# Kernel optimization log

Measured on AMD Instinct MI355X. Metric: run time of the kernel, lower is better.

The kernel has to match this reference:

```python
import jax, jax.numpy as jnp
import numpy as np

EMBED_DIM = 768
NUM_HEADS = 12
KEY_DIM = EMBED_DIM // NUM_HEADS
B, S = 2, 2048

def _xavier(key, shape):
    # xavier_uniform over last-two dims (fan_in = shape[-2], fan_out = shape[-1])
    fan_in, fan_out = shape[-2], shape[-1]
    limit = jnp.sqrt(6.0 / (fan_in + fan_out)).astype(jnp.float32)
    return jax.random.uniform(key, shape, jnp.float32, -limit, limit)

def setup_inputs() -> dict:
    key = jax.random.key(0)
    kq, kk, kv, kwq, kwk, kwv, kw, km = jax.random.split(key, 8)
    q = jax.random.normal(kq, (B, S, EMBED_DIM), jnp.float32)
    k = jax.random.normal(kk, (B, S, EMBED_DIM), jnp.float32)
    v = jax.random.normal(kv, (B, S, EMBED_DIM), jnp.float32)
    # per-head projection weights stacked: [H, E, Dk]
    Wq = _xavier(kwq, (NUM_HEADS, EMBED_DIM, KEY_DIM))
    Wk = _xavier(kwk, (NUM_HEADS, EMBED_DIM, KEY_DIM))
    Wv = _xavier(kwv, (NUM_HEADS, EMBED_DIM, KEY_DIM))
    W = _xavier(kw, (EMBED_DIM, EMBED_DIM))
    mask = jax.random.randint(km, (B, 1, S, S), 0, 2).astype(jnp.int32)
    return {"q": q, "k": k, "v": v, "mask": mask, "Wq": Wq, "Wk": Wk, "Wv": Wv, "W": W}

def reference(q, k, v, mask, Wq, Wk, Wv, W):
    scale = 1.0 / jnp.sqrt(jnp.asarray(KEY_DIM, q.dtype))
    Q = jnp.einsum('bse,hed->bhsd', q, Wq)  # [B,H,S,Dk]
    K = jnp.einsum('bse,hed->bhsd', k, Wk)
    V = jnp.einsum('bse,hed->bhsd', v, Wv)
    Z = jnp.einsum('bhsd,bhtd->bhst', Q, K) * scale  # [B,H,S,S]
    Z = jnp.where(mask == 0, jnp.asarray(-1e9, Z.dtype), Z)
    score = jax.nn.softmax(Z, axis=-1)
    out = jnp.einsum('bhst,bhtd->bhsd', score, V)  # [B,H,S,Dk]
    # concat heads along last dim (head order = list order)
    concat = out.transpose(0, 2, 1, 3).reshape(q.shape[0], q.shape[1], EMBED_DIM)
    return concat @ W
```

## Files before the change

### kernel.cpp

```cpp
#include <hip/hip_runtime.h>
#include <stdint.h>

typedef uint16_t u16;
typedef __attribute__((ext_vector_type(8))) short bf16x8;
typedef __attribute__((ext_vector_type(4))) float f32x4;
typedef __attribute__((ext_vector_type(16))) float f32x16;

#define EMB 768
#define NH 12
#define DK 64
#define BB 2
#define SS 2048
#define SCL 0.1803368801111244f
#define M0  24.0f

__device__ __forceinline__ u16 f2bf(float x) {
  union { float f; uint32_t u; } v; v.f = x;
  uint32_t r = v.u + 0x7fffu + ((v.u >> 16) & 1u);
  return (u16)(r >> 16);
}

__device__ __forceinline__ uint32_t pk2(float a, float b) {
  uint32_t d;
  asm("v_cvt_pk_bf16_f32 %0, %1, %2" : "=v"(d) : "v"(a), "v"(b));
  return d;
}

__device__ __forceinline__ void gld16(const u16* g, u16* l) {
  __builtin_amdgcn_global_load_lds((const __attribute__((address_space(1))) void*)g,
                                   (__attribute__((address_space(3))) void*)l, 16, 0, 0);
}

__global__ void pack_all(const float* __restrict__ wq, const float* __restrict__ wk,
                         const float* __restrict__ wv, const float* __restrict__ w,
                         const int* __restrict__ mask,
                         u16* __restrict__ wqkvT, u16* __restrict__ wT,
                         uint64_t* __restrict__ bits) {
  uint32_t tl = blockIdx.x * 256 + threadIdx.x;
  const uint32_t WTOT = 4u * EMB * EMB;
  if (tl < WTOT) {
    int z = tl / (EMB * EMB);
    int t = tl - z * (EMB * EMB);
    int n = t / EMB, e = t - n * EMB;
    if (z < 3) {
      const float* src = z == 0 ? wq : (z == 1 ? wk : wv);
      float vv = src[((n >> 6) * EMB + e) * DK + (n & 63)];
      if (z == 0) vv *= SCL;
      wqkvT[(size_t)z * EMB * EMB + t] = f2bf(vv);
    } else {
      wT[t] = f2bf(w[e * EMB + n]);
    }
  } else {
    uint32_t widx = tl - WTOT;
    uint32_t wv64 = widx >> 6;
    uint32_t lane = widx & 63;
    uint32_t b  = wv64 >> 12;
    uint32_t qg = (wv64 >> 6) & 63;
    uint32_t tg = wv64 & 63;
    uint32_t c = lane & 31, hi = lane >> 5;
    const int* mp = mask + (((size_t)b * 2048 + qg * 32 + c) * 2048 + tg * 32 + hi * 4);
    int4 q0 = *(const int4*)mp;
    int4 q1 = *(const int4*)(mp + 8);
    int4 q2 = *(const int4*)(mp + 16);
    int4 q3 = *(const int4*)(mp + 24);
    uint64_t* wout = bits + (size_t)wv64 * 16;
    unsigned long long ball;
#define BAL(u, arr)                                                   \
    ball = __ballot(arr.x != 0); if (lane == 0) wout[u * 4 + 0] = ball; \
    ball = __ballot(arr.y != 0); if (lane == 0) wout[u * 4 + 1] = ball; \
    ball = __ballot(arr.z != 0); if (lane == 0) wout[u * 4 + 2] = ball; \
    ball = __ballot(arr.w != 0); if (lane == 0) wout[u * 4 + 3] = ball;
    BAL(0, q0) BAL(1, q1) BAL(2, q2) BAL(3, q3)
#undef BAL
  }
}

#define GEMM_MFMA_BODY(Ab, Bb)                                                  \
    bf16x8 af[4], bfr[4];                                                       \
    _Pragma("unroll")                                                           \
    for (int i = 0; i < 4; ++i)                                                 \
      af[i] = *(const bf16x8*)((Ab) + (wr * 64 + i * 16 + c) * 32 + quad * 8);  \
    _Pragma("unroll")                                                           \
    for (int j = 0; j < 4; ++j)                                                 \
      bfr[j] = *(const bf16x8*)((Bb) + (wc * 64 + j * 16 + c) * 32 + quad * 8); \
    _Pragma("unroll")                                                           \
    for (int i = 0; i < 4; ++i)                                                 \
      _Pragma("unroll")                                                         \
      for (int j = 0; j < 4; ++j)                                               \
        acc[i][j] = __builtin_amdgcn_mfma_f32_16x16x32_bf16(af[i], bfr[j], acc[i][j], 0, 0, 0);

__device__ __forceinline__ void gemm_f32A_pipe(const float* __restrict__ A,
                                               const u16* __restrict__ Bt, int Kdim,
                                               int m0, int n0, u16* As, u16* Bs,
                                               f32x4 (&acc)[4][4]) {
  const int tid = threadIdx.x;
  const int lane = tid & 63, quad = lane >> 4, c = lane & 15;
  const int wr = (tid >> 6) >> 1, wc = (tid >> 6) & 1;
  float4 a0[2], a1[2];
#define LOAD_A(kk)                                                     \
  _Pragma("unroll")                                                    \
  for (int p = 0; p < 2; ++p) {                                        \
    int idx = (p * 256 + tid) * 8;                                     \
    const float* src = A + (size_t)(m0 + (idx >> 5)) * Kdim + (kk) + (idx & 31); \
    a0[p] = *(const float4*)src; a1[p] = *(const float4*)(src + 4);    \
  }
#define ISSUE_B(kk, buf)                                               \
  _Pragma("unroll")                                                    \
  for (int r = 0; r < 2; ++r) {                                        \
    int bo = r * 4096 + tid * 16;                                      \
    gld16(Bt + (size_t)(n0 + (bo >> 6)) * Kdim + (kk) + ((bo & 63) >> 1), \
          Bs + (buf) * 4096 + (bo >> 1));                              \
  }
  LOAD_A(0); ISSUE_B(0, 0);
  for (int kk = 0; kk < Kdim; kk += 32) {
    const int buf = (kk >> 5) & 1;
#pragma unroll
    for (int p = 0; p < 2; ++p) {
      int idx = (p * 256 + tid) * 8;
      uint4 pkv = { pk2(a0[p].x, a0[p].y), pk2(a0[p].z, a0[p].w),
                    pk2(a1[p].x, a1[p].y), pk2(a1[p].z, a1[p].w) };
      *(uint4*)(As + buf * 4096 + (idx >> 5) * 32 + (idx & 31)) = pkv;
    }
    __syncthreads();
    if (kk + 32 < Kdim) { LOAD_A(kk + 32); ISSUE_B(kk + 32, buf ^ 1); }
    const u16* Ab = As + buf * 4096;
    const u16* Bb = Bs + buf * 4096;
    GEMM_MFMA_BODY(Ab, Bb)
  }
#undef LOAD_A
#undef ISSUE_B
}

__device__ __forceinline__ void gemm_bf16A_pipe(const u16* __restrict__ A,
                                                const u16* __restrict__ Bt, int Kdim,
                                                int m0, int n0, u16* As, u16* Bs,
                                                f32x4 (&acc)[4][4]) {
  const int tid = threadIdx.x;
  const int lane = tid & 63, quad = lane >> 4, c = lane & 15;
  const int wr = (tid >> 6) >> 1, wc = (tid >> 6) & 1;
#define ISSUE_AB(kk, buf)                                              \
  _Pragma("unroll")                                                    \
  for (int r = 0; r < 2; ++r) {                                        \
    int bo = r * 4096 + tid * 16;                                      \
    gld16(A  + (size_t)(m0 + (bo >> 6)) * Kdim + (kk) + ((bo & 63) >> 1), \
          As + (buf) * 4096 + (bo >> 1));                              \
    gld16(Bt + (size_t)(n0 + (bo >> 6)) * Kdim + (kk) + ((bo & 63) >> 1), \
          Bs + (buf) * 4096 + (bo >> 1));                              \
  }
  ISSUE_AB(0, 0);
  for (int kk = 0; kk < Kdim; kk += 32) {
    const int buf = (kk >> 5) & 1;
    __syncthreads();
    if (kk + 32 < Kdim) { ISSUE_AB(kk + 32, buf ^ 1); }
    const u16* Ab = As + buf * 4096;
    const u16* Bb = Bs + buf * 4096;
    GEMM_MFMA_BODY(Ab, Bb)
  }
#undef ISSUE_AB
}

__launch_bounds__(256, 3)
__global__ void gemm_qkv(const float* __restrict__ q, const float* __restrict__ k,
                         const float* __restrict__ v, const u16* __restrict__ wt3,
                         u16* __restrict__ Qp, u16* __restrict__ Kp, u16* __restrict__ Vt) {
  __shared__ u16 As[2 * 128 * 32];
  __shared__ u16 Bs[2 * 128 * 32];
  const int z = blockIdx.z;
  const float* A = z == 0 ? q : (z == 1 ? k : v);
  const u16* Bt = wt3 + (size_t)z * EMB * EMB;
  const int m0 = blockIdx.y * 128, n0 = blockIdx.x * 128;
  f32x4 acc[4][4];
  const f32x4 fz = {0.f, 0.f, 0.f, 0.f};
#pragma unroll
  for (int i = 0; i < 4; ++i)
#pragma unroll
    for (int j = 0; j < 4; ++j) acc[i][j] = fz;
  gemm_f32A_pipe(A, Bt, EMB, m0, n0, As, Bs, acc);
  const int tid = threadIdx.x, lane = tid & 63, quad = lane >> 4, c = lane & 15;
  const int wr = (tid >> 6) >> 1, wc = (tid >> 6) & 1;
  if (z < 2) {
    u16* C = z == 0 ? Qp : Kp;
#pragma unroll
    for (int i = 0; i < 4; ++i)
#pragma unroll
      for (int j = 0; j < 4; ++j) {
        int row = m0 + wr * 64 + i * 16 + quad * 4;
        int col = n0 + wc * 64 + j * 16 + c;
#pragma unroll
        for (int r = 0; r < 4; r += 2) {
          uint32_t d = pk2(acc[i][j][r], acc[i][j][r + 1]);
          C[(size_t)(row + r) * EMB + col] = (u16)d;
          C[(size_t)(row + r + 1) * EMB + col] = (u16)(d >> 16);
        }
      }
  } else {
#pragma unroll
    for (int i = 0; i < 4; ++i)
#pragma unroll
      for (int j = 0; j < 4; ++j) {
        int row = m0 + wr * 64 + i * 16 + quad * 4;
        int col = n0 + wc * 64 + j * 16 + c;
        int b = row >> 11, s = row & 2047;
        int h = col >> 6, d = col & 63;
        uint2 pk = { pk2(acc[i][j][0], acc[i][j][1]), pk2(acc[i][j][2], acc[i][j][3]) };
        *(uint2*)(Vt + ((size_t)(b * NH + h) * DK + d) * SS + s) = pk;
      }
  }
}

__launch_bounds__(256, 3)
__global__ void gemm_out(const u16* __restrict__ A, const u16* __restrict__ Bt,
                         float* __restrict__ C) {
  __shared__ u16 As[2 * 128 * 32];
  __shared__ u16 Bs[2 * 128 * 32];
  const int m0 = blockIdx.y * 128, n0 = blockIdx.x * 128;
  f32x4 acc[4][4];
  const f32x4 fz = {0.f, 0.f, 0.f, 0.f};
#pragma unroll
  for (int i = 0; i < 4; ++i)
#pragma unroll
    for (int j = 0; j < 4; ++j) acc[i][j] = fz;
  gemm_bf16A_pipe(A, Bt, EMB, m0, n0, As, Bs, acc);
  const int tid = threadIdx.x, lane = tid & 63, quad = lane >> 4, c = lane & 15;
  const int wr = (tid >> 6) >> 1, wc = (tid >> 6) & 1;
#pragma unroll
  for (int i = 0; i < 4; ++i)
#pragma unroll
    for (int j = 0; j < 4; ++j)
#pragma unroll
      for (int r = 0; r < 4; ++r) {
        int row = m0 + wr * 64 + i * 16 + quad * 4 + r;
        int col = n0 + wc * 64 + j * 16 + c;
        C[(size_t)row * EMB + col] = acc[i][j][r];
      }
}

__launch_bounds__(512, 4)
__global__ void attn(const u16* __restrict__ Qp, const u16* __restrict__ Kp,
                     const u16* __restrict__ Vt, const uint64_t* __restrict__ MW,
                     u16* __restrict__ AO) {
  __shared__ __align__(16) u16 sm[2 * 128 * 72 + 2 * 64 * 136];
  u16* Ks0 = sm;
  u16* Vs0 = sm + 2 * 128 * 72;

  const int tid = threadIdx.x, lane = tid & 63;
  const int c = lane & 31, hi = lane >> 5;
  const int w = tid >> 6;
  const int wq2 = w >> 2, th = w & 3;

  const int wid = blockIdx.x;
  const int xcd = wid & 7, slot = wid >> 3;
  const int bh = xcd + 8 * (slot >> 5);
  const int mtile = slot & 31;
  const int b = bh / NH, h = bh - b * NH;
  const int m0 = mtile * 64;

  const size_t qkbase = (size_t)b * SS * EMB + (size_t)h * DK;
  const size_t vtbase = (size_t)bh * DK * SS;

  bf16x8 aq[4];
  {
    const u16* qr = Qp + qkbase + (size_t)(m0 + wq2 * 32 + c) * EMB + hi * 8;
    aq[0] = *(const bf16x8*)(qr);
    aq[1] = *(const bf16x8*)(qr + 16);
    aq[2] = *(const bf16x8*)(qr + 32);
    aq[3] = *(const bf16x8*)(qr + 48);
  }

  const int srK = tid >> 2, scK = (tid & 3) * 16;
  const int srV = tid >> 3, scV = (tid & 7) * 16;
  const u16* gK = Kp + qkbase + (size_t)srK * EMB + scK;
  const u16* gV = Vt + vtbase + (size_t)srV * SS + scV;
  bf16x8 kr0, kr1, vr0, vr1;
#define LOADKV(t0) {                                             \
    const u16* gk_ = gK + (size_t)(t0) * EMB;                    \
    kr0 = *(const bf16x8*)gk_; kr1 = *(const bf16x8*)(gk_ + 8);  \
    const u16* gv_ = gV + (t0);                                  \
    vr0 = *(const bf16x8*)gv_; vr1 = *(const bf16x8*)(gv_ + 8); }
#define STOREKV(buf) {                                           \
    u16* ks_ = Ks0 + (buf) * (128 * 72) + srK * 72 + scK;        \
    *(bf16x8*)ks_ = kr0; *(bf16x8*)(ks_ + 8) = kr1;              \
    u16* vs_ = Vs0 + (buf) * (64 * 136) + srV * 136 + scV;       \
    *(bf16x8*)vs_ = vr0; *(bf16x8*)(vs_ + 8) = vr1; }

  const int thu = __builtin_amdgcn_readfirstlane(th);
  const int qgu = __builtin_amdgcn_readfirstlane(mtile * 2 + wq2);
  const uint64_t* mwb = MW + (((size_t)b * 64 + qgu) * 64) * 16 + thu * 16;
#define LOADMSK(m, it) {                                         \
    const uint64_t* mp_ = mwb + (size_t)(it) * 64;               \
    _Pragma("unroll")                                            \
    for (int r_ = 0; r_ < 16; ++r_) m[r_] = mp_[r_]; }

  float fNEG = -1e9f, fM0 = -M0;
  float lr = 0.f;
  f32x16 o0, o1;
#pragma unroll
  for (int r_ = 0; r_ < 16; ++r_) { o0[r_] = 0.f; o1[r_] = 0.f; }

  uint64_t mA[16], mB[16];
  LOADKV(0); LOADMSK(mA, 0);

#define BODY(it, buf, mc, mn) {                                                   \
    STOREKV(buf);                                                                 \
    __syncthreads();                                                              \
    if ((it) < 15) { LOADKV(((it) + 1) * 128); LOADMSK(mn, (it) + 1); }           \
     \
    f32x16 s;                                                                     \
    _Pragma("unroll")                                                             \
    for (int r_ = 0; r_ < 16; ++r_) {                                             \
      float t_;                                                                   \
      asm("v_cndmask_b32 %0, %1, %2, %3"                                          \
          : "=v"(t_) : "v"(fNEG), "v"(fM0), "s"(mc[r_]));                         \
      s[r_] = t_;                                                                 \
    }                                                                             \
                                          \
    const u16* kb_ = Ks0 + (buf) * (128 * 72) + (th * 32 + c) * 72 + hi * 8;      \
    _Pragma("unroll")                                                             \
    for (int ks_ = 0; ks_ < 4; ++ks_) {                                           \
      bf16x8 kf_ = *(const bf16x8*)(kb_ + ks_ * 16);                              \
      s = __builtin_amdgcn_mfma_f32_32x32x16_bf16(kf_, aq[ks_], s, 0, 0, 0);      \
    }                                                                             \
                               \
    _Pragma("unroll")                                                             \
    for (int r_ = 0; r_ < 16; ++r_) s[r_] = __builtin_amdgcn_exp2f(s[r_]);        \
    lr += ((s[0] + s[1]) + (s[2] + s[3])) + ((s[4] + s[5]) + (s[6] + s[7]))       \
        + ((s[8] + s[9]) + (s[10] + s[11])) + ((s[12] + s[13]) + (s[14] + s[15]));\
                      \
    uint32_t x0 = pk2(s[0], s[1]),  x1 = pk2(s[2], s[3]);                         \
    uint32_t y0 = pk2(s[4], s[5]),  y1 = pk2(s[6], s[7]);                         \
    uint32_t z0 = pk2(s[8], s[9]),  z1 = pk2(s[10], s[11]);                       \
    uint32_t w0 = pk2(s[12], s[13]), w1 = pk2(s[14], s[15]);                      \
    asm("v_permlane32_swap_b32 %0, %1" : "+v"(x0), "+v"(y0));                     \
    asm("v_permlane32_swap_b32 %0, %1" : "+v"(x1), "+v"(y1));                     \
    asm("v_permlane32_swap_b32 %0, %1" : "+v"(z0), "+v"(w0));                     \
    asm("v_permlane32_swap_b32 %0, %1" : "+v"(z1), "+v"(w1));                     \
    bf16x8 pa0, pa1;                                                              \
    { union { uint32_t u[4]; bf16x8 v; } cv;                                      \
      cv.u[0] = x0; cv.u[1] = x1; cv.u[2] = y0; cv.u[3] = y1; pa0 = cv.v;         \
      cv.u[0] = z0; cv.u[1] = z1; cv.u[2] = w0; cv.u[3] = w1; pa1 = cv.v; }       \
                                  \
    const u16* vb_ = Vs0 + (buf) * (64 * 136) + c * 136 + th * 32 + hi * 8;       \
    {                                                                             \
      bf16x8 vf_;                                                                 \
      vf_ = *(const bf16x8*)(vb_);                                                \
      o0 = __builtin_amdgcn_mfma_f32_32x32x16_bf16(vf_, pa0, o0, 0, 0, 0);        \
      vf_ = *(const bf16x8*)(vb_ + 16);                                           \
      o0 = __builtin_amdgcn_mfma_f32_32x32x16_bf16(vf_, pa1, o0, 0, 0, 0);        \
      vf_ = *(const bf16x8*)(vb_ + 32 * 136);                                     \
      o1 = __builtin_amdgcn_mfma_f32_32x32x16_bf16(vf_, pa0, o1, 0, 0, 0);        \
      vf_ = *(const bf16x8*)(vb_ + 32 * 136 + 16);                                \
      o1 = __builtin_amdgcn_mfma_f32_32x32x16_bf16(vf_, pa1, o1, 0, 0, 0);        \
    } }

  for (int i2 = 0; i2 < 8; ++i2) {
    BODY(i2 * 2,     0, mA, mB)
    BODY(i2 * 2 + 1, 1, mB, mA)
  }
#undef BODY
#undef LOADKV
#undef STOREKV
#undef LOADMSK

  lr += __shfl_xor(lr, 32);
  __syncthreads();
  float* Of = (float*)sm;
  float* Lf = (float*)sm + 4 * 64 * 65;
  {
    int row = wq2 * 32 + c;
#pragma unroll
    for (int r_ = 0; r_ < 16; ++r_) {
      int d = (r_ & 3) + 8 * (r_ >> 2) + 4 * hi;
      Of[(th * 64 + row) * 65 + d]      = o0[r_];
      Of[(th * 64 + row) * 65 + 32 + d] = o1[r_];
    }
    if (hi == 0) Lf[row * 4 + th] = lr;
  }
  __syncthreads();
  {
    int qrow = tid >> 3, d0 = (tid & 7) * 8;
    float lt = Lf[qrow * 4 + 0] + Lf[qrow * 4 + 1] + Lf[qrow * 4 + 2] + Lf[qrow * 4 + 3];
    float inv = 1.f / fmaxf(lt, 1e-20f);
    float acc[8];
#pragma unroll
    for (int e = 0; e < 8; ++e) acc[e] = 0.f;
#pragma unroll
    for (int t_ = 0; t_ < 4; ++t_)
#pragma unroll
      for (int e = 0; e < 8; ++e) acc[e] += Of[(t_ * 64 + qrow) * 65 + d0 + e];
    uint32_t dw[4];
#pragma unroll
    for (int e = 0; e < 4; ++e) dw[e] = pk2(acc[2 * e] * inv, acc[2 * e + 1] * inv);
    *(uint4*)(AO + qkbase + (size_t)(m0 + qrow) * EMB + d0) = *(uint4*)dw;
  }
}

extern "C" void kernel_launch(void* const* d_in, const int* in_sizes, int n_in,
                              void* d_out, int out_size, void* d_ws, size_t ws_size,
                              hipStream_t stream) {
  const float* q  = (const float*)d_in[0];
  const float* k  = (const float*)d_in[1];
  const float* v  = (const float*)d_in[2];
  const int* mask = (const int*)d_in[3];
  const float* Wq = (const float*)d_in[4];
  const float* Wk = (const float*)d_in[5];
  const float* Wv = (const float*)d_in[6];
  const float* W  = (const float*)d_in[7];
  float* out = (float*)d_out;

  u16* Kp = (u16*)d_out;
  u16* Vt = (u16*)d_out + 3145728;

  u16* ws    = (u16*)d_ws;
  u16* Qp    = ws;
  u16* WqkvT = ws + 3145728;
  u16* WT    = ws + 3145728 + 1769472;
  uint64_t* mb64 = (uint64_t*)(ws + 5505024);
  u16* AO = Qp;

  pack_all<<<dim3(11264), 256, 0, stream>>>(Wq, Wk, Wv, W, mask, WqkvT, WT, mb64);
  gemm_qkv<<<dim3(6, 32, 3), 256, 0, stream>>>(q, k, v, WqkvT, Qp, Kp, Vt);
  attn<<<dim3(768), 512, 0, stream>>>(Qp, Kp, Vt, mb64, AO);
  gemm_out<<<dim3(6, 32), 256, 0, stream>>>(AO, WT, out);
}
```

Before: 230.4 us.

## Shrink GEMM M-tile to 64 and remap blocks to XCD-grouped panels

The QKV and output projection GEMMs now use 64x128 tiles instead of 128x128, doubling block count to 1152 and 384 so more of the CUs are busy, with occupancy hint raised to 4. Block IDs are remapped so each XCD handles contiguous row panels across all N tiles, which is meant to improve L2 reuse of the A panel. The cost is more B-tile reloads per output and less MFMA work per LDS load.

New measurement: 226.9 us. About the same (-1.5%).

```diff
diff --git a/kernel.cpp b/kernel.cpp
--- a/kernel.cpp
+++ b/kernel.cpp
@@ -75,34 +75,33 @@
   }
 }
 
-#define GEMM_MFMA_BODY(Ab, Bb)                                                  \
-    bf16x8 af[4], bfr[4];                                                       \
+#define GEMM_MFMA_BODY64(Ab, Bb)                                                \
+    bf16x8 af[2], bfr[4];                                                       \
     _Pragma("unroll")                                                           \
-    for (int i = 0; i < 4; ++i)                                                 \
-      af[i] = *(const bf16x8*)((Ab) + (wr * 64 + i * 16 + c) * 32 + quad * 8);  \
+    for (int i = 0; i < 2; ++i)                                                 \
+      af[i] = *(const bf16x8*)((Ab) + (wr * 32 + i * 16 + c) * 32 + quad * 8);  \
     _Pragma("unroll")                                                           \
     for (int j = 0; j < 4; ++j)                                                 \
       bfr[j] = *(const bf16x8*)((Bb) + (wc * 64 + j * 16 + c) * 32 + quad * 8); \
     _Pragma("unroll")                                                           \
-    for (int i = 0; i < 4; ++i)                                                 \
+    for (int i = 0; i < 2; ++i)                                                 \
       _Pragma("unroll")                                                         \
       for (int j = 0; j < 4; ++j)                                               \
         acc[i][j] = __builtin_amdgcn_mfma_f32_16x16x32_bf16(af[i], bfr[j], acc[i][j], 0, 0, 0);
 
-__device__ __forceinline__ void gemm_f32A_pipe(const float* __restrict__ A,
-                                               const u16* __restrict__ Bt, int Kdim,
-                                               int m0, int n0, u16* As, u16* Bs,
-                                               f32x4 (&acc)[4][4]) {
+__device__ __forceinline__ void gemm_f32A_pipe64(const float* __restrict__ A,
+                                                 const u16* __restrict__ Bt, int Kdim,
+                                                 int m0, int n0, u16* As, u16* Bs,
+                                                 f32x4 (&acc)[2][4]) {
   const int tid = threadIdx.x;
   const int lane = tid & 63, quad = lane >> 4, c = lane & 15;
   const int wr = (tid >> 6) >> 1, wc = (tid >> 6) & 1;
-  float4 a0[2], a1[2];
+  const int arow = tid >> 2, acol = (tid & 3) * 8;
+  float4 a0, a1;
 #define LOAD_A(kk)                                                     \
-  _Pragma("unroll")                                                    \
-  for (int p = 0; p < 2; ++p) {                                        \
-    int idx = (p * 256 + tid) * 8;                                     \
-    const float* src = A + (size_t)(m0 + (idx >> 5)) * Kdim + (kk) + (idx & 31); \
-    a0[p] = *(const float4*)src; a1[p] = *(const float4*)(src + 4);    \
+  {                                                                    \
+    const float* src = A + (size_t)(m0 + arow) * Kdim + (kk) + acol;   \
+    a0 = *(const float4*)src; a1 = *(const float4*)(src + 4);          \
   }
 #define ISSUE_B(kk, buf)                                               \
   _Pragma("unroll")                                                    \
@@ -114,77 +113,81 @@
   LOAD_A(0); ISSUE_B(0, 0);
   for (int kk = 0; kk < Kdim; kk += 32) {
     const int buf = (kk >> 5) & 1;
-#pragma unroll
-    for (int p = 0; p < 2; ++p) {
-      int idx = (p * 256 + tid) * 8;
-      uint4 pkv = { pk2(a0[p].x, a0[p].y), pk2(a0[p].z, a0[p].w),
-                    pk2(a1[p].x, a1[p].y), pk2(a1[p].z, a1[p].w) };
-      *(uint4*)(As + buf * 4096 + (idx >> 5) * 32 + (idx & 31)) = pkv;
+    {
+      uint4 pkv = { pk2(a0.x, a0.y), pk2(a0.z, a0.w),
+                    pk2(a1.x, a1.y), pk2(a1.z, a1.w) };
+      *(uint4*)(As + buf * 2048 + arow * 32 + acol) = pkv;
     }
     __syncthreads();
     if (kk + 32 < Kdim) { LOAD_A(kk + 32); ISSUE_B(kk + 32, buf ^ 1); }
-    const u16* Ab = As + buf * 4096;
+    const u16* Ab = As + buf * 2048;
     const u16* Bb = Bs + buf * 4096;
-    GEMM_MFMA_BODY(Ab, Bb)
+    GEMM_MFMA_BODY64(Ab, Bb)
   }
 #undef LOAD_A
 #undef ISSUE_B
 }
 
-__device__ __forceinline__ void gemm_bf16A_pipe(const u16* __restrict__ A,
-                                                const u16* __restrict__ Bt, int Kdim,
-                                                int m0, int n0, u16* As, u16* Bs,
-                                                f32x4 (&acc)[4][4]) {
+__device__ __forceinline__ void gemm_bf16A_pipe64(const u16* __restrict__ A,
+                                                  const u16* __restrict__ Bt, int Kdim,
+                                                  int m0, int n0, u16* As, u16* Bs,
+                                                  f32x4 (&acc)[2][4]) {
   const int tid = threadIdx.x;
   const int lane = tid & 63, quad = lane >> 4, c = lane & 15;
   const int wr = (tid >> 6) >> 1, wc = (tid >> 6) & 1;
 #define ISSUE_AB(kk, buf)                                              \
-  _Pragma("unroll")                                                    \
-  for (int r = 0; r < 2; ++r) {                                        \
-    int bo = r * 4096 + tid * 16;                                      \
-    gld16(A  + (size_t)(m0 + (bo >> 6)) * Kdim + (kk) + ((bo & 63) >> 1), \
-          As + (buf) * 4096 + (bo >> 1));                              \
-    gld16(Bt + (size_t)(n0 + (bo >> 6)) * Kdim + (kk) + ((bo & 63) >> 1), \
-          Bs + (buf) * 4096 + (bo >> 1));                              \
+  {                                                                    \
+    gld16(A + (size_t)(m0 + (tid >> 2)) * Kdim + (kk) + (tid & 3) * 8, \
+          As + (buf) * 2048 + tid * 8);                                \
+    _Pragma("unroll")                                                  \
+    for (int r = 0; r < 2; ++r) {                                      \
+      int bo = r * 4096 + tid * 16;                                    \
+      gld16(Bt + (size_t)(n0 + (bo >> 6)) * Kdim + (kk) + ((bo & 63) >> 1), \
+            Bs + (buf) * 4096 + (bo >> 1));                            \
+    }                                                                  \
   }
   ISSUE_AB(0, 0);
   for (int kk = 0; kk < Kdim; kk += 32) {
     const int buf = (kk >> 5) & 1;
     __syncthreads();
     if (kk + 32 < Kdim) { ISSUE_AB(kk + 32, buf ^ 1); }
-    const u16* Ab = As + buf * 4096;
+    const u16* Ab = As + buf * 2048;
     const u16* Bb = Bs + buf * 4096;
-    GEMM_MFMA_BODY(Ab, Bb)
+    GEMM_MFMA_BODY64(Ab, Bb)
   }
 #undef ISSUE_AB
 }
 
-__launch_bounds__(256, 3)
+__launch_bounds__(256, 4)
 __global__ void gemm_qkv(const float* __restrict__ q, const float* __restrict__ k,
                          const float* __restrict__ v, const u16* __restrict__ wt3,
                          u16* __restrict__ Qp, u16* __restrict__ Kp, u16* __restrict__ Vt) {
-  __shared__ u16 As[2 * 128 * 32];
+  __shared__ u16 As[2 * 64 * 32];
   __shared__ u16 Bs[2 * 128 * 32];
-  const int z = blockIdx.z;
+  const int id = blockIdx.x;
+  const int xcd = id & 7, s = id >> 3;
+  const int panel = xcd * 24 + s / 6;
+  const int ntile = s - (s / 6) * 6;
+  const int z = panel >> 6, mt = panel & 63;
+  const int m0 = mt * 64, n0 = ntile * 128;
   const float* A = z == 0 ? q : (z == 1 ? k : v);
   const u16* Bt = wt3 + (size_t)z * EMB * EMB;
-  const int m0 = blockIdx.y * 128, n0 = blockIdx.x * 128;
-  f32x4 acc[4][4];
+  f32x4 acc[2][4];
   const f32x4 fz = {0.f, 0.f, 0.f, 0.f};
 #pragma unroll
-  for (int i = 0; i < 4; ++i)
+  for (int i = 0; i < 2; ++i)
 #pragma unroll
     for (int j = 0; j < 4; ++j) acc[i][j] = fz;
-  gemm_f32A_pipe(A, Bt, EMB, m0, n0, As, Bs, acc);
+  gemm_f32A_pipe64(A, Bt, EMB, m0, n0, As, Bs, acc);
   const int tid = threadIdx.x, lane = tid & 63, quad = lane >> 4, c = lane & 15;
   const int wr = (tid >> 6) >> 1, wc = (tid >> 6) & 1;
   if (z < 2) {
     u16* C = z == 0 ? Qp : Kp;
 #pragma unroll
-    for (int i = 0; i < 4; ++i)
+    for (int i = 0; i < 2; ++i)
 #pragma unroll
       for (int j = 0; j < 4; ++j) {
-        int row = m0 + wr * 64 + i * 16 + quad * 4;
+        int row = m0 + wr * 32 + i * 16 + quad * 4;
         int col = n0 + wc * 64 + j * 16 + c;
 #pragma unroll
         for (int r = 0; r < 4; r += 2) {
@@ -195,41 +198,45 @@
       }
   } else {
 #pragma unroll
-    for (int i = 0; i < 4; ++i)
+    for (int i = 0; i < 2; ++i)
 #pragma unroll
       for (int j = 0; j < 4; ++j) {
-        int row = m0 + wr * 64 + i * 16 + quad * 4;
+        int row = m0 + wr * 32 + i * 16 + quad * 4;
         int col = n0 + wc * 64 + j * 16 + c;
-        int b = row >> 11, s = row & 2047;
+        int b = row >> 11, ss = row & 2047;
         int h = col >> 6, d = col & 63;
         uint2 pk = { pk2(acc[i][j][0], acc[i][j][1]), pk2(acc[i][j][2], acc[i][j][3]) };
-        *(uint2*)(Vt + ((size_t)(b * NH + h) * DK + d) * SS + s) = pk;
+        *(uint2*)(Vt + ((size_t)(b * NH + h) * DK + d) * SS + ss) = pk;
       }
   }
 }
 
-__launch_bounds__(256, 3)
+__launch_bounds__(256, 4)
 __global__ void gemm_out(const u16* __restrict__ A, const u16* __restrict__ Bt,
                          float* __restrict__ C) {
-  __shared__ u16 As[2 * 128 * 32];
+  __shared__ u16 As[2 * 64 * 32];
   __shared__ u16 Bs[2 * 128 * 32];
-  const int m0 = blockIdx.y * 128, n0 = blockIdx.x * 128;
-  f32x4 acc[4][4];
+  const int id = blockIdx.x;
+  const int xcd = id & 7, s = id >> 3;
+  const int panel = xcd * 8 + s / 6;
+  const int ntile = s - (s / 6) * 6;
+  const int m0 = panel * 64, n0 = ntile * 128;
+  f32x4 acc[2][4];
   const f32x4 fz = {0.f, 0.f, 0.f, 0.f};
 #pragma unroll
-  for (int i = 0; i < 4; ++i)
+  for (int i = 0; i < 2; ++i)
 #pragma unroll
     for (int j = 0; j < 4; ++j) acc[i][j] = fz;
-  gemm_bf16A_pipe(A, Bt, EMB, m0, n0, As, Bs, acc);
+  gemm_bf16A_pipe64(A, Bt, EMB, m0, n0, As, Bs, acc);
   const int tid = threadIdx.x, lane = tid & 63, quad = lane >> 4, c = lane & 15;
   const int wr = (tid >> 6) >> 1, wc = (tid >> 6) & 1;
 #pragma unroll
-  for (int i = 0; i < 4; ++i)
+  for (int i = 0; i < 2; ++i)
 #pragma unroll
     for (int j = 0; j < 4; ++j)
 #pragma unroll
       for (int r = 0; r < 4; ++r) {
-        int row = m0 + wr * 64 + i * 16 + quad * 4 + r;
+        int row = m0 + wr * 32 + i * 16 + quad * 4 + r;
         int col = n0 + wc * 64 + j * 16 + c;
         C[(size_t)row * EMB + col] = acc[i][j][r];
       }
@@ -418,7 +425,7 @@
   u16* AO = Qp;
 
   pack_all<<<dim3(11264), 256, 0, stream>>>(Wq, Wk, Wv, W, mask, WqkvT, WT, mb64);
-  gemm_qkv<<<dim3(6, 32, 3), 256, 0, stream>>>(q, k, v, WqkvT, Qp, Kp, Vt);
+  gemm_qkv<<<dim3(1152), 256, 0, stream>>>(q, k, v, WqkvT, Qp, Kp, Vt);
   attn<<<dim3(768), 512, 0, stream>>>(Qp, Kp, Vt, mb64, AO);
-  gemm_out<<<dim3(6, 32), 256, 0, stream>>>(AO, WT, out);
-}
+  gemm_out<<<dim3(384), 256, 0, stream>>>(AO, WT, out);
+}
```
